# Kernel tuning notes

Hardware: AMD Instinct MI355X
Metric: run time of the kernel (lower is better)

Reference implementation:

```python
import jax, jax.numpy as jnp
import numpy as np

B, T, D, H = 64, 512, 1024, 1024


def setup_inputs() -> dict:
    key = jax.random.key(0)
    k1, k2, k3, k4, k5, k6 = jax.random.split(key, 6)
    feature = jax.random.normal(k1, (B, T, D), dtype=jnp.float32)
    # lengths sorted descending (pack_padded_sequence enforce_sorted=True); max == T
    lens = jnp.sort(jax.random.randint(k2, (B,), 1, T + 1))[::-1]
    seq_len = lens.at[0].set(T).astype(jnp.int32)
    s = 1.0 / np.sqrt(H)
    W_ih = jax.random.uniform(k3, (4 * H, D), jnp.float32, -s, s)
    W_hh = jax.random.uniform(k4, (4 * H, H), jnp.float32, -s, s)
    b_ih = jax.random.uniform(k5, (4 * H,), jnp.float32, -s, s)
    b_hh = jax.random.uniform(k6, (4 * H,), jnp.float32, -s, s)
    return {"feature": feature, "W_ih": W_ih, "W_hh": W_hh,
            "b_ih": b_ih, "b_hh": b_hh, "seq_len": seq_len}


def _lstm(feature, W_ih, W_hh, b_ih, b_hh, seq_len):
    Bb, Tt, _ = feature.shape
    Hh = W_hh.shape[1]
    # precompute input contributions for all steps: [B,T,4H] -> [T,B,4H]
    x_gates = jnp.einsum('btd,gd->btg', feature, W_ih) + (b_ih + b_hh)
    x_gates = jnp.transpose(x_gates, (1, 0, 2))
    # valid-step mask per timestep: [T,B]
    mask = (jnp.arange(Tt)[:, None] < seq_len[None, :])

    def step(carry, inp):
        h, c = carry
        xg, m = inp  # [B,4H], [B]
        gates = xg + h @ W_hh.T
        i, f, g, o = jnp.split(gates, 4, axis=-1)  # PyTorch gate order i,f,g,o
        i = jax.nn.sigmoid(i)
        f = jax.nn.sigmoid(f)
        g = jnp.tanh(g)
        o = jax.nn.sigmoid(o)
        c_new = f * c + i * g
        h_new = o * jnp.tanh(c_new)
        m = m[:, None]
        h = jnp.where(m, h_new, h)  # packed semantics: state frozen past length
        c = jnp.where(m, c_new, c)
        out = jnp.where(m, h_new, 0.0)  # pad_packed_sequence pads with zeros
        return (h, c), out

    h0 = jnp.zeros((Bb, Hh), feature.dtype)
    c0 = jnp.zeros((Bb, Hh), feature.dtype)
    _, outs = jax.lax.scan(step, (h0, c0), (x_gates, mask))
    return jnp.transpose(outs, (1, 0, 2))  # [B,T,H]


def reference(feature, W_ih, W_hh, b_ih, b_hh, seq_len):
    return _lstm(feature, W_ih, W_hh, b_ih, b_hh, seq_len)
```

## Files before the change

### kernel.cpp

```cpp
#include <hip/hip_runtime.h>
#include <stdint.h>

typedef unsigned short ushort_t;
typedef unsigned long long ull_t;
typedef __attribute__((ext_vector_type(8))) short short8;
typedef __attribute__((ext_vector_type(2))) unsigned long long ull2;
typedef __attribute__((ext_vector_type(4))) float f32x4;
typedef __attribute__((ext_vector_type(4))) float float4v;
typedef __attribute__((ext_vector_type(4))) unsigned short ushort4v;
typedef __attribute__((ext_vector_type(4))) unsigned int uint4v;

#define NB 64
#define NT 512
#define ND 1024
#define NHH 1024
#define NG 4096

__device__ __forceinline__ ushort_t f2bf(float x) {
    uint32_t u = __builtin_bit_cast(uint32_t, x);
    u += 0x7fffu + ((u >> 16) & 1u);
    return (ushort_t)(u >> 16);
}
__device__ __forceinline__ float bf2f(ushort_t b) {
    uint32_t u = ((uint32_t)b) << 16;
    return __builtin_bit_cast(float, u);
}
__device__ __forceinline__ float fsigmoid(float x) { return 1.f / (1.f + __expf(-x)); }
__device__ __forceinline__ float ftanh(float x) {
    float ax = __builtin_fabsf(x);
    float e = __expf(-2.f * ax);
    float r = (1.f - e) / (1.f + e);
    return x < 0.f ? -r : r;
}
__device__ __forceinline__ void xg_store(float* p, float v) { *p = v; }
__device__ __forceinline__ void xg_store(ushort_t* p, float v) { *p = f2bf(v); }
__device__ __forceinline__ float4v xg_load4(const float4v* p) { return *p; }
__device__ __forceinline__ float4v xg_load4(const ushort4v* p) {
    ushort4v u = *p;
    float4v r = { bf2f(u[0]), bf2f(u[1]), bf2f(u[2]), bf2f(u[3]) };
    return r;
}

__global__ __launch_bounds__(256) void k_prep(
    const float* __restrict__ feat, const float* __restrict__ wih,
    const float* __restrict__ whh,
    ushort_t* __restrict__ featb, ushort_t* __restrict__ wihb,
    ushort_t* __restrict__ whhb, ushort_t* __restrict__ hbuf,
    int* __restrict__ cnt)
{
    const size_t NF = (size_t)NB * NT * ND / 4;
    const size_t NW = (size_t)NG * ND / 4;
    const size_t NHB = (size_t)2 * 65536 * 2 / 16;
    size_t total = NF + 2 * NW + NHB;
    size_t stride = (size_t)gridDim.x * blockDim.x;
    for (size_t i = (size_t)blockIdx.x * blockDim.x + threadIdx.x; i < total; i += stride) {
        if (i < NF) {
            float4v v = ((const float4v*)feat)[i];
            ushort4v o = { f2bf(v[0]), f2bf(v[1]), f2bf(v[2]), f2bf(v[3]) };
            ((ushort4v*)featb)[i] = o;
        } else if (i < NF + NW) {
            size_t j = i - NF;
            size_t row = j >> 8, kc = j & 255;
            size_t rowp = ((row & 1023) << 2) | (row >> 10);
            float4v v = ((const float4v*)wih)[j];
            ushort4v o = { f2bf(v[0]), f2bf(v[1]), f2bf(v[2]), f2bf(v[3]) };
            ((ushort4v*)wihb)[rowp * 256 + kc] = o;
        } else if (i < NF + 2 * NW) {
            size_t j = i - NF - NW;
            float4v v = ((const float4v*)whh)[j];
            ushort4v o = { f2bf(v[0]), f2bf(v[1]), f2bf(v[2]), f2bf(v[3]) };
            ((ushort4v*)whhb)[j] = o;
        } else {
            size_t j = i - NF - 2 * NW;
            uint4v z = { 0u, 0u, 0u, 0u };
            ((uint4v*)hbuf)[j] = z;
        }
    }
    if (blockIdx.x < 4) cnt[blockIdx.x * 256 + threadIdx.x] = 0;
}

template <typename XGT>
__global__ __launch_bounds__(256) void k_gemm(
    const ushort_t* __restrict__ Ab,
    const ushort_t* __restrict__ Bb,
    const float* __restrict__ bih, const float* __restrict__ bhh,
    const int* __restrict__ slenp, XGT* __restrict__ xg)
{
    int bid = blockIdx.x;
    int panel = bid >> 8;
    int qq = bid & 255;
    int mt = (panel << 3) | (qq & 7);
    int nt = qq >> 3;
    int m0 = mt << 7, n0 = nt << 7;
    int b = m0 >> 9;
    int t0 = m0 & 511;
    int sl = slenp[b];
    if (t0 >= sl) return;

    __shared__ ushort_t ldsA[8 * 129 * 8];
    __shared__ ushort_t ldsB[8 * 129 * 8];
    short8* sA = (short8*)ldsA;
    short8* sB = (short8*)ldsB;
    const short8* gA = (const short8*)Ab + (size_t)m0 * 128;
    const short8* gB = (const short8*)Bb + (size_t)n0 * 128;

    int tid = threadIdx.x;
    int wave = tid >> 6, lane = tid & 63;
    int wm = (wave >> 1) << 6;
    int wn = (wave & 1) << 6;
    int fl = lane & 15, fq = lane >> 4;

    f32x4 acc[4][4];
#pragma unroll
    for (int i = 0; i < 4; i++)
#pragma unroll
        for (int j = 0; j < 4; j++) { f32x4 z = {0.f, 0.f, 0.f, 0.f}; acc[i][j] = z; }

    int row_[4], kb_[4];
#pragma unroll
    for (int u = 0; u < 4; u++) { int c = u * 256 + tid; row_[u] = c >> 3; kb_[u] = c & 7; }

    for (int k0 = 0; k0 < 128; k0 += 8) {
        short8 va[4], vb[4];
#pragma unroll
        for (int u = 0; u < 4; u++) {
            va[u] = gA[(size_t)row_[u] * 128 + k0 + kb_[u]];
            vb[u] = gB[(size_t)row_[u] * 128 + k0 + kb_[u]];
        }
        __syncthreads();
#pragma unroll
        for (int u = 0; u < 4; u++) {
            sA[kb_[u] * 129 + row_[u]] = va[u];
            sB[kb_[u] * 129 + row_[u]] = vb[u];
        }
        __syncthreads();
#pragma unroll
        for (int ks = 0; ks < 2; ks++) {
            short8 af[4], bf[4];
#pragma unroll
            for (int i = 0; i < 4; i++) {
                af[i] = sA[(ks * 4 + fq) * 129 + wm + i * 16 + fl];
                bf[i] = sB[(ks * 4 + fq) * 129 + wn + i * 16 + fl];
            }
#pragma unroll
            for (int i = 0; i < 4; i++)
#pragma unroll
                for (int j = 0; j < 4; j++)
                    acc[i][j] = __builtin_amdgcn_mfma_f32_16x16x32_bf16(af[i], bf[j], acc[i][j], 0, 0, 0);
        }
    }
#pragma unroll
    for (int j = 0; j < 4; j++) {
        int rp = n0 + wn + j * 16 + fl;
        int bi = ((rp & 3) << 10) | (rp >> 2);
        float bv = bih[bi] + bhh[bi];
#pragma unroll
        for (int i = 0; i < 4; i++) {
#pragma unroll
            for (int r = 0; r < 4; r++) {
                int m = wm + i * 16 + fq * 4 + r;
                int t = t0 + m;
                if (t < sl)
                    xg_store(&xg[((size_t)t * 64 + b) * 4096 + rp], acc[i][j][r] + bv);
            }
        }
    }
}

template <typename XG4>
__global__ __launch_bounds__(256, 1) void k_rec(
    const ushort_t* __restrict__ whhb, const XG4* __restrict__ xg4,
    const int* __restrict__ slenp, ushort_t* __restrict__ hbuf,
    float* __restrict__ out, int* __restrict__ cnt)
{
    const int tid = threadIdx.x;
    const int ks = tid >> 6, lane = tid & 63;
    const int wg = blockIdx.x;
    const int mb = wg >> 6;
    const int j0 = (wg & 63) << 4;
    const int nn = lane & 15, q = lane >> 4;

    short8 wfrag[4][8];
    {
        const short8* w8 = (const short8*)whhb;
#pragma unroll
        for (int g = 0; g < 4; g++) {
            const short8* wp = w8 + (size_t)(g * NHH + j0 + nn) * 128 + ks * 32;
#pragma unroll
            for (int u = 0; u < 8; u++) wfrag[g][u] = wp[u * 4 + q];
        }
    }
    const int eb = tid >> 4, ej = tid & 15;
    const int b_g = (mb << 4) + eb;
    const int j_g = j0 + ej;
    const int slen = slenp[b_g];
    const int blk_len = slenp[mb << 4];
    const int ab = (mb << 4) + nn;

    int* gcnt = cnt + ((wg >> 4) * 32);
    int* root = cnt + 512;
    int* flag = cnt + 640 + ((wg >> 4) * 16);
    const bool leader = ((wg & 15) == 0);

    __shared__ float red[4 * 16 * 84];

    float c_st = 0.f, h_st = 0.f, hv_prev = 0.f;

#pragma unroll 1
    for (int t = 0; t < NT; ++t) {
        if (t > 0) out[((size_t)b_g * NT + (t - 1)) * 1024 + j_g] = hv_prev;
        float4v xv = { 0.f, 0.f, 0.f, 0.f };
        if (t < slen) xv = xg_load4(&xg4[((size_t)t * 64 + b_g) * 1024 + j_g]);

        bool blk_active = (t < blk_len);
        if (blk_active) {
            const ull_t* hb8 = (const ull_t*)(hbuf + (size_t)(t & 1) * 65536);
            ull_t raw[16];
#pragma unroll
            for (int u = 0; u < 8; u++) {
                size_t ch = ((size_t)((ks * 32 + u * 4 + q) * 64 + ab)) * 2;
                raw[2 * u]     = __hip_atomic_load(&hb8[ch],     __ATOMIC_RELAXED, __HIP_MEMORY_SCOPE_AGENT);
                raw[2 * u + 1] = __hip_atomic_load(&hb8[ch + 1], __ATOMIC_RELAXED, __HIP_MEMORY_SCOPE_AGENT);
            }
            f32x4 acc[4];
#pragma unroll
            for (int g = 0; g < 4; g++) { f32x4 z = {0.f, 0.f, 0.f, 0.f}; acc[g] = z; }
#pragma unroll
            for (int u = 0; u < 8; u++) {
                ull2 p; p[0] = raw[2 * u]; p[1] = raw[2 * u + 1];
                short8 af = __builtin_bit_cast(short8, p);
#pragma unroll
                for (int g = 0; g < 4; g++)
                    acc[g] = __builtin_amdgcn_mfma_f32_16x16x32_bf16(af, wfrag[g][u], acc[g], 0, 0, 0);
            }
            __syncthreads();
#pragma unroll
            for (int g = 0; g < 4; g++)
                *(f32x4*)&red[g * 1344 + nn * 84 + ks * 20 + q * 4] = acc[g];
            __syncthreads();
        }
        float hv = 0.f;
        if (t < slen) {
            float s[4];
#pragma unroll
            for (int g = 0; g < 4; g++) {
                const float* rp = &red[g * 1344 + ej * 84 + eb];
                s[g] = (rp[0] + rp[20]) + (rp[40] + rp[60]);
            }
            float ip = s[0] + xv[0];
            float fp = s[1] + xv[1];
            float gp = s[2] + xv[2];
            float op = s[3] + xv[3];
            float i_s = fsigmoid(ip), f_s = fsigmoid(fp);
            float g_t = ftanh(gp), o_s = fsigmoid(op);
            float cn = __builtin_fmaf(f_s, c_st, i_s * g_t);
            c_st = cn;
            h_st = o_s * ftanh(cn);
            hv = h_st;
        }
        hv_prev = hv;
        __hip_atomic_store(&hbuf[(size_t)((t + 1) & 1) * 65536 +
                                 (size_t)((j_g >> 3) * 64 + b_g) * 8 + (j_g & 7)],
                           f2bf(h_st), __ATOMIC_RELAXED, __HIP_MEMORY_SCOPE_AGENT);
        if (t != NT - 1) {
            asm volatile("s_waitcnt vmcnt(0)" ::: "memory");
            __syncthreads();
            if (tid == 0) {
                int old = __hip_atomic_fetch_add(gcnt, 1, __ATOMIC_RELAXED, __HIP_MEMORY_SCOPE_AGENT);
                if ((old & 15) == 15)
                    __hip_atomic_fetch_add(root, 1, __ATOMIC_RELAXED, __HIP_MEMORY_SCOPE_AGENT);
                const int target = (t + 1) << 4;
                if (leader) {
                    while (__hip_atomic_load(root, __ATOMIC_RELAXED, __HIP_MEMORY_SCOPE_AGENT) < target)
                        __builtin_amdgcn_s_sleep(2);
                    __hip_atomic_store(flag, t + 1, __ATOMIC_RELAXED, __HIP_MEMORY_SCOPE_AGENT);
                } else {
                    while (__hip_atomic_load(flag, __ATOMIC_RELAXED, __HIP_MEMORY_SCOPE_AGENT) < t + 1)
                        __builtin_amdgcn_s_sleep(2);
                }
            }
            __syncthreads();
        }
    }
    out[((size_t)b_g * NT + (NT - 1)) * 1024 + j_g] = hv_prev;
}

extern "C" void kernel_launch(void* const* d_in, const int* in_sizes, int n_in,
                              void* d_out, int out_size, void* d_ws, size_t ws_size,
                              hipStream_t stream)
{
    const float* feat = (const float*)d_in[0];
    const float* wih  = (const float*)d_in[1];
    const float* whh  = (const float*)d_in[2];
    const float* bih  = (const float*)d_in[3];
    const float* bhh  = (const float*)d_in[4];
    const int*   sl   = (const int*)d_in[5];
    float* out = (float*)d_out;
    char* ws = (char*)d_ws;

    size_t off = 0;
    auto take = [&](size_t bytes) -> size_t {
        size_t o = off; off += (bytes + 255) & ~(size_t)255; return o;
    };
    size_t o_featb = take((size_t)NB * NT * ND * 2);
    size_t o_wihb  = take((size_t)NG * ND * 2);
    size_t o_whhb  = take((size_t)NG * ND * 2);
    size_t o_hbuf  = take((size_t)2 * 65536 * 2);
    size_t o_cnt   = take(4096);
    size_t o_xg    = off;

    ushort_t* featb = (ushort_t*)(ws + o_featb);
    ushort_t* wihb  = (ushort_t*)(ws + o_wihb);
    ushort_t* whhb  = (ushort_t*)(ws + o_whhb);
    ushort_t* hbuf  = (ushort_t*)(ws + o_hbuf);
    int* cnt        = (int*)(ws + o_cnt);

    k_prep<<<2048, 256, 0, stream>>>(feat, wih, whh, featb, wihb, whhb, hbuf, cnt);

    size_t xg_elems = (size_t)NT * NB * NG;
    bool f32xg = (o_xg + xg_elems * 4) <= ws_size;
    if (f32xg) {
        float* xg = (float*)(ws + o_xg);
        k_gemm<float><<<8192, 256, 0, stream>>>(featb, wihb, bih, bhh, sl, xg);
        k_rec<float4v><<<256, 256, 0, stream>>>(whhb, (const float4v*)xg, sl, hbuf, out, cnt);
    } else {
        ushort_t* xg = (ushort_t*)(ws + o_xg);
        k_gemm<ushort_t><<<8192, 256, 0, stream>>>(featb, wihb, bih, bhh, sl, xg);
        k_rec<ushort4v><<<256, 256, 0, stream>>>(whhb, (const ushort4v*)xg, sl, hbuf, out, cnt);
    }
}
```

Measured before the change: 2.644 ms.

## Per-batch-block barriers, early exit at block length, async LDS loads in GEMM

The recurrent kernel now synchronizes only the 64 workgroups that share a batch block, with an 8-way sub-barrier tree, instead of one global barrier across all workgroups. Each batch block stops stepping at its own maximum length and zero-fills the remaining outputs. The next step's input-gate values are prefetched one step ahead. The input GEMM switches to direct global-to-LDS async copies with an XOR swizzle and a 64-wide K chunk, replacing register-staged transposed stores. Together these aim to cut barrier latency, skip padded timesteps, and reduce GEMM load overhead, at the cost of a larger counter area and more complex synchronization.

```diff
diff --git a/kernel.cpp b/kernel.cpp
--- a/kernel.cpp
+++ b/kernel.cpp
@@ -39,6 +39,11 @@
     ushort4v u = *p;
     float4v r = { bf2f(u[0]), bf2f(u[1]), bf2f(u[2]), bf2f(u[3]) };
     return r;
+}
+__device__ __forceinline__ void async_cp16(const ushort_t* g, ushort_t* s) {
+    __builtin_amdgcn_global_load_lds(
+        (const __attribute__((address_space(1))) uint32_t*)g,
+        (__attribute__((address_space(3))) uint32_t*)s, 16, 0, 0);
 }
 
 __global__ __launch_bounds__(256) void k_prep(
@@ -76,7 +81,7 @@
             ((uint4v*)hbuf)[j] = z;
         }
     }
-    if (blockIdx.x < 4) cnt[blockIdx.x * 256 + threadIdx.x] = 0;
+    if (blockIdx.x < 16) cnt[blockIdx.x * 256 + threadIdx.x] = 0;
 }
 
 template <typename XGT>
@@ -97,12 +102,12 @@
     int sl = slenp[b];
     if (t0 >= sl) return;
 
-    __shared__ ushort_t ldsA[8 * 129 * 8];
-    __shared__ ushort_t ldsB[8 * 129 * 8];
-    short8* sA = (short8*)ldsA;
-    short8* sB = (short8*)ldsB;
-    const short8* gA = (const short8*)Ab + (size_t)m0 * 128;
-    const short8* gB = (const short8*)Bb + (size_t)n0 * 128;
+    __shared__ short8 ldsA8[1024];
+    __shared__ short8 ldsB8[1024];
+    ushort_t* ldsA = (ushort_t*)ldsA8;
+    ushort_t* ldsB = (ushort_t*)ldsB8;
+    const ushort_t* gA = Ab + (size_t)m0 * 1024;
+    const ushort_t* gB = Bb + (size_t)n0 * 1024;
 
     int tid = threadIdx.x;
     int wave = tid >> 6, lane = tid & 63;
@@ -116,31 +121,34 @@
 #pragma unroll
         for (int j = 0; j < 4; j++) { f32x4 z = {0.f, 0.f, 0.f, 0.f}; acc[i][j] = z; }
 
-    int row_[4], kb_[4];
-#pragma unroll
-    for (int u = 0; u < 4; u++) { int c = u * 256 + tid; row_[u] = c >> 3; kb_[u] = c & 7; }
-
-    for (int k0 = 0; k0 < 128; k0 += 8) {
-        short8 va[4], vb[4];
+    int srow_[4], skb_[4];
+#pragma unroll
+    for (int u = 0; u < 4; u++) {
+        int s = u * 256 + tid;
+        srow_[u] = s >> 3;
+        skb_[u] = (s & 7) ^ (srow_[u] & 7);
+    }
+
+    for (int k0 = 0; k0 < 1024; k0 += 64) {
+        if (k0) __syncthreads();
 #pragma unroll
         for (int u = 0; u < 4; u++) {
-            va[u] = gA[(size_t)row_[u] * 128 + k0 + kb_[u]];
-            vb[u] = gB[(size_t)row_[u] * 128 + k0 + kb_[u]];
+            ushort_t* sa = ldsA + (size_t)(u * 256 + wave * 64) * 8;
+            ushort_t* sb = ldsB + (size_t)(u * 256 + wave * 64) * 8;
+            async_cp16(gA + (size_t)srow_[u] * 1024 + k0 + skb_[u] * 8, sa);
+            async_cp16(gB + (size_t)srow_[u] * 1024 + k0 + skb_[u] * 8, sb);
         }
         __syncthreads();
 #pragma unroll
-        for (int u = 0; u < 4; u++) {
-            sA[kb_[u] * 129 + row_[u]] = va[u];
-            sB[kb_[u] * 129 + row_[u]] = vb[u];
-        }
-        __syncthreads();
-#pragma unroll
         for (int ks = 0; ks < 2; ks++) {
+            int kc = ks * 4 + fq;
             short8 af[4], bf[4];
 #pragma unroll
             for (int i = 0; i < 4; i++) {
-                af[i] = sA[(ks * 4 + fq) * 129 + wm + i * 16 + fl];
-                bf[i] = sB[(ks * 4 + fq) * 129 + wn + i * 16 + fl];
+                int ra = wm + i * 16 + fl;
+                int rb = wn + i * 16 + fl;
+                af[i] = ldsA8[ra * 8 + (kc ^ (ra & 7))];
+                bf[i] = ldsB8[rb * 8 + (kc ^ (rb & 7))];
             }
 #pragma unroll
             for (int i = 0; i < 4; i++)
@@ -177,7 +185,8 @@
     const int ks = tid >> 6, lane = tid & 63;
     const int wg = blockIdx.x;
     const int mb = wg >> 6;
-    const int j0 = (wg & 63) << 4;
+    const int mem = wg & 63;
+    const int j0 = mem << 4;
     const int nn = lane & 15, q = lane >> 4;
 
     short8 wfrag[4][8];
@@ -197,48 +206,49 @@
     const int blk_len = slenp[mb << 4];
     const int ab = (mb << 4) + nn;
 
-    int* gcnt = cnt + ((wg >> 4) * 32);
-    int* root = cnt + 512;
-    int* flag = cnt + 640 + ((wg >> 4) * 16);
-    const bool leader = ((wg & 15) == 0);
+    int* base    = cnt + mb * 512;
+    int* subcnt  = base + (mem >> 3) * 16;
+    int* root    = base + 256;
+    int* subflag = base + 272 + (mem >> 3) * 16;
+    const bool subleader = ((mem & 7) == 0);
 
     __shared__ float red[4 * 16 * 84];
 
     float c_st = 0.f, h_st = 0.f, hv_prev = 0.f;
+    float4v xv = { 0.f, 0.f, 0.f, 0.f };
+    if (0 < slen) xv = xg_load4(&xg4[(size_t)b_g * 1024 + j_g]);
 
 #pragma unroll 1
-    for (int t = 0; t < NT; ++t) {
+    for (int t = 0; t < blk_len; ++t) {
         if (t > 0) out[((size_t)b_g * NT + (t - 1)) * 1024 + j_g] = hv_prev;
-        float4v xv = { 0.f, 0.f, 0.f, 0.f };
-        if (t < slen) xv = xg_load4(&xg4[((size_t)t * 64 + b_g) * 1024 + j_g]);
-
-        bool blk_active = (t < blk_len);
-        if (blk_active) {
-            const ull_t* hb8 = (const ull_t*)(hbuf + (size_t)(t & 1) * 65536);
-            ull_t raw[16];
-#pragma unroll
-            for (int u = 0; u < 8; u++) {
-                size_t ch = ((size_t)((ks * 32 + u * 4 + q) * 64 + ab)) * 2;
-                raw[2 * u]     = __hip_atomic_load(&hb8[ch],     __ATOMIC_RELAXED, __HIP_MEMORY_SCOPE_AGENT);
-                raw[2 * u + 1] = __hip_atomic_load(&hb8[ch + 1], __ATOMIC_RELAXED, __HIP_MEMORY_SCOPE_AGENT);
-            }
-            f32x4 acc[4];
-#pragma unroll
-            for (int g = 0; g < 4; g++) { f32x4 z = {0.f, 0.f, 0.f, 0.f}; acc[g] = z; }
-#pragma unroll
-            for (int u = 0; u < 8; u++) {
-                ull2 p; p[0] = raw[2 * u]; p[1] = raw[2 * u + 1];
-                short8 af = __builtin_bit_cast(short8, p);
-#pragma unroll
-                for (int g = 0; g < 4; g++)
-                    acc[g] = __builtin_amdgcn_mfma_f32_16x16x32_bf16(af, wfrag[g][u], acc[g], 0, 0, 0);
-            }
-            __syncthreads();
+        float4v nxv = { 0.f, 0.f, 0.f, 0.f };
+        if (t + 1 < slen) nxv = xg_load4(&xg4[((size_t)(t + 1) * 64 + b_g) * 1024 + j_g]);
+
+        const ull_t* hb8 = (const ull_t*)(hbuf + (size_t)(t & 1) * 65536);
+        ull_t raw[16];
+#pragma unroll
+        for (int u = 0; u < 8; u++) {
+            size_t ch = ((size_t)((ks * 32 + u * 4 + q) * 64 + ab)) * 2;
+            raw[2 * u]     = __hip_atomic_load(&hb8[ch],     __ATOMIC_RELAXED, __HIP_MEMORY_SCOPE_AGENT);
+            raw[2 * u + 1] = __hip_atomic_load(&hb8[ch + 1], __ATOMIC_RELAXED, __HIP_MEMORY_SCOPE_AGENT);
+        }
+        f32x4 acc[4];
+#pragma unroll
+        for (int g = 0; g < 4; g++) { f32x4 z = {0.f, 0.f, 0.f, 0.f}; acc[g] = z; }
+#pragma unroll
+        for (int u = 0; u < 8; u++) {
+            ull2 p; p[0] = raw[2 * u]; p[1] = raw[2 * u + 1];
+            short8 af = __builtin_bit_cast(short8, p);
 #pragma unroll
             for (int g = 0; g < 4; g++)
-                *(f32x4*)&red[g * 1344 + nn * 84 + ks * 20 + q * 4] = acc[g];
-            __syncthreads();
-        }
+                acc[g] = __builtin_amdgcn_mfma_f32_16x16x32_bf16(af, wfrag[g][u], acc[g], 0, 0, 0);
+        }
+        __syncthreads();
+#pragma unroll
+        for (int g = 0; g < 4; g++)
+            *(f32x4*)&red[g * 1344 + nn * 84 + ks * 20 + q * 4] = acc[g];
+        __syncthreads();
+
         float hv = 0.f;
         if (t < slen) {
             float s[4];
@@ -262,27 +272,30 @@
         __hip_atomic_store(&hbuf[(size_t)((t + 1) & 1) * 65536 +
                                  (size_t)((j_g >> 3) * 64 + b_g) * 8 + (j_g & 7)],
                            f2bf(h_st), __ATOMIC_RELAXED, __HIP_MEMORY_SCOPE_AGENT);
-        if (t != NT - 1) {
+        xv = nxv;
+        if (t + 1 < blk_len) {
             asm volatile("s_waitcnt vmcnt(0)" ::: "memory");
             __syncthreads();
             if (tid == 0) {
-                int old = __hip_atomic_fetch_add(gcnt, 1, __ATOMIC_RELAXED, __HIP_MEMORY_SCOPE_AGENT);
-                if ((old & 15) == 15)
+                int old = __hip_atomic_fetch_add(subcnt, 1, __ATOMIC_RELAXED, __HIP_MEMORY_SCOPE_AGENT);
+                if ((old & 7) == 7)
                     __hip_atomic_fetch_add(root, 1, __ATOMIC_RELAXED, __HIP_MEMORY_SCOPE_AGENT);
-                const int target = (t + 1) << 4;
-                if (leader) {
+                const int target = (t + 1) << 3;
+                if (subleader) {
                     while (__hip_atomic_load(root, __ATOMIC_RELAXED, __HIP_MEMORY_SCOPE_AGENT) < target)
                         __builtin_amdgcn_s_sleep(2);
-                    __hip_atomic_store(flag, t + 1, __ATOMIC_RELAXED, __HIP_MEMORY_SCOPE_AGENT);
+                    __hip_atomic_store(subflag, t + 1, __ATOMIC_RELAXED, __HIP_MEMORY_SCOPE_AGENT);
                 } else {
-                    while (__hip_atomic_load(flag, __ATOMIC_RELAXED, __HIP_MEMORY_SCOPE_AGENT) < t + 1)
+                    while (__hip_atomic_load(subflag, __ATOMIC_RELAXED, __HIP_MEMORY_SCOPE_AGENT) < t + 1)
                         __builtin_amdgcn_s_sleep(2);
                 }
             }
             __syncthreads();
         }
     }
-    out[((size_t)b_g * NT + (NT - 1)) * 1024 + j_g] = hv_prev;
+    out[((size_t)b_g * NT + (blk_len - 1)) * 1024 + j_g] = hv_prev;
+    for (int t = blk_len; t < NT; ++t)
+        out[((size_t)b_g * NT + t) * 1024 + j_g] = 0.f;
 }
 
 extern "C" void kernel_launch(void* const* d_in, const int* in_sizes, int n_in,
@@ -306,7 +319,7 @@
     size_t o_wihb  = take((size_t)NG * ND * 2);
     size_t o_whhb  = take((size_t)NG * ND * 2);
     size_t o_hbuf  = take((size_t)2 * 65536 * 2);
-    size_t o_cnt   = take(4096);
+    size_t o_cnt   = take(16384);
     size_t o_xg    = off;
 
     ushort_t* featb = (ushort_t*)(ws + o_featb);
```

Result: no change. 2.608 ms (-1.4%).
